# Kernel optimization log

Hardware: AMD Instinct MI355X
Metric: run time of the kernel (lower is better)

The kernel has to match this reference:

```python
import jax, jax.numpy as jnp
import numpy as np

N_NODES = 100000
N_EDGES = 3200000
IN_DIM = 128
HID = 128
K = 20  # n_gaussians


def gcn_conv(x, src, dst, W, b, n_nodes):
    """PyG GCNConv: add self-loops, symmetric normalization, linear transform.
    out = D^{-1/2} (A + I) D^{-1/2} (x @ W) + b, where D is degree of A+I.
    """
    h = x @ W  # [N, out_dim]
    # degree on A + I (self-loop contributes 1 to every node)
    deg = jax.ops.segment_sum(jnp.ones_like(dst, dtype=h.dtype), dst,
                              num_segments=n_nodes) + 1.0
    dis = jax.lax.rsqrt(deg)  # deg >= 1, safe
    norm = dis[src] * dis[dst]  # [E]
    # gather -> scale -> scatter-add (edges), plus self-loop term dis_i^2 * h_i
    agg = jax.ops.segment_sum(h[src] * norm[:, None], dst,
                              num_segments=n_nodes)
    agg = agg + h * (dis * dis)[:, None]
    return agg + b


def setup_inputs() -> dict:
    key = jax.random.key(0)
    ks = jax.random.split(key, 12)
    x = jax.random.normal(ks[0], (N_NODES, IN_DIM), dtype=jnp.float32)
    edge_index = jax.random.randint(ks[1], (2, N_EDGES), 0, N_NODES, dtype=jnp.int32)
    s = 1.0 / np.sqrt(HID)
    W1 = jax.random.uniform(ks[2], (IN_DIM, HID), jnp.float32, -s, s)
    b1 = jnp.zeros((HID,), jnp.float32)
    W2 = jax.random.uniform(ks[3], (HID, HID), jnp.float32, -s, s)
    b2 = jnp.zeros((HID,), jnp.float32)
    pi_W = jax.random.uniform(ks[4], (HID, K), jnp.float32, -s, s)
    pi_b = jnp.zeros((K,), jnp.float32)
    mu_W = jax.random.uniform(ks[5], (HID, K), jnp.float32, -s, s)
    mu_b = jnp.zeros((K,), jnp.float32)
    ls_W = jax.random.uniform(ks[6], (HID, K), jnp.float32, -s, s)
    ls_b = jnp.zeros((K,), jnp.float32)
    return {"x": x, "edge_index": edge_index, "W1": W1, "b1": b1,
            "W2": W2, "b2": b2, "pi_W": pi_W, "pi_b": pi_b,
            "mu_W": mu_W, "mu_b": mu_b, "ls_W": ls_W, "ls_b": ls_b}


def reference(x, edge_index, W1, b1, W2, b2, pi_W, pi_b, mu_W, mu_b, ls_W, ls_b):
    src, dst = edge_index[0], edge_index[1]
    n = x.shape[0]
    h = jax.nn.relu(gcn_conv(x, src, dst, W1, b1, n))
    h = jax.nn.relu(gcn_conv(h, src, dst, W2, b2, n))
    pi = jax.nn.softmax(h @ pi_W + pi_b, axis=1)
    mu = h @ mu_W + mu_b
    log_sigma = h @ ls_W + ls_b
    return (pi, mu, log_sigma)
```

## Files before the change

### kernel.cpp

```cpp
#include <hip/hip_runtime.h>
#include <hip/hip_fp16.h>
#include <cstdint>
#include <cstddef>

#define IN_DIM 128
#define HID    128
#define NG     20
#define T      4096
#define MAXB   400

typedef _Float16 half8 __attribute__((ext_vector_type(8)));
typedef _Float16 half4 __attribute__((ext_vector_type(4)));
typedef float    f32x4 __attribute__((ext_vector_type(4)));

__global__ void zero_ints(int* __restrict__ a, int n) {
  int i = blockIdx.x * blockDim.x + threadIdx.x;
  if (i < n) a[i] = 0;
}

__global__ __launch_bounds__(256) void binsort1(const int* __restrict__ src,
    const int* __restrict__ dst, int* __restrict__ tmp, int* __restrict__ bofs,
    int* __restrict__ bintot, int NBC, int E) {
  __shared__ int lhist[MAXB];
  __shared__ int lscan[512];
  __shared__ int lcur[MAXB];
  __shared__ int sbuf[T];
  int tid = threadIdx.x;
  int tile0 = blockIdx.x * T;
  int m = E - tile0; if (m > T) m = T;

  for (int i = tid; i < NBC; i += 256) lhist[i] = 0;
  __syncthreads();

  int dreg[16];
#pragma unroll
  for (int j = 0; j < 16; ++j) {
    int idx = j * 256 + tid;
    dreg[j] = -1;
    if (idx < m) {
      int d = dst[tile0 + idx];
      dreg[j] = d;
      atomicAdd(&lhist[d >> 8], 1);
    }
  }
  __syncthreads();

  int v0 = (tid < NBC) ? lhist[tid] : 0;
  int v1 = (256 + tid < NBC) ? lhist[256 + tid] : 0;
  lscan[tid] = v0; lscan[256 + tid] = v1;
  __syncthreads();
  for (int o = 1; o < 512; o <<= 1) {
    int a0 = (tid >= o) ? lscan[tid - o] : 0;
    int a1 = (256 + tid >= o) ? lscan[256 + tid - o] : 0;
    __syncthreads();
    lscan[tid] += a0; lscan[256 + tid] += a1;
    __syncthreads();
  }
  if (tid < NBC)       lcur[tid]       = lscan[tid] - v0;
  if (256 + tid < NBC) lcur[256 + tid] = lscan[256 + tid] - v1;
  __syncthreads();

  int ST = NBC + 1;
  for (int i = tid; i < NBC; i += 256) bofs[(size_t)blockIdx.x * ST + i] = lcur[i];
  if (tid == 0) bofs[(size_t)blockIdx.x * ST + NBC] = m;
  for (int i = tid; i < NBC; i += 256)
    if (lhist[i]) atomicAdd(&bintot[i], lhist[i]);
  __syncthreads();

#pragma unroll
  for (int j = 0; j < 16; ++j) {
    int idx = j * 256 + tid;
    if (idx < m) {
      int d = dreg[j];
      int s = src[tile0 + idx];
      int slot = atomicAdd(&lcur[d >> 8], 1);
      sbuf[slot] = ((d & 255) << 17) | s;
    }
  }
  __syncthreads();

  int nv = m >> 2;
  int4* out4 = (int4*)(tmp + tile0);
  const int4* sb4 = (const int4*)sbuf;
  for (int i = tid; i < nv; i += 256) out4[i] = sb4[i];
  for (int i = (nv << 2) + tid; i < m; i += 256) tmp[tile0 + i] = sbuf[i];
}

__global__ __launch_bounds__(512) void binscan(const int* __restrict__ bintot,
                                               int* __restrict__ binbase, int NBC) {
  __shared__ int s[512];
  int tid = threadIdx.x;
  int v = (tid < NBC) ? bintot[tid] : 0;
  s[tid] = v;
  __syncthreads();
  for (int o = 1; o < 512; o <<= 1) {
    int t = (tid >= o) ? s[tid - o] : 0;
    __syncthreads();
    s[tid] += t;
    __syncthreads();
  }
  if (tid < NBC) binbase[tid] = s[tid] - v;
}

__global__ __launch_bounds__(512) void binsort2(const int* __restrict__ tmp,
    const int* __restrict__ bofs, const int* __restrict__ binbase,
    int* __restrict__ csrc, int* __restrict__ cnt, float* __restrict__ dis,
    int* __restrict__ offs, int NBC, int nblk, int N) {
  __shared__ int lcnt[256];
  __shared__ int lsc[256];
  __shared__ int lcur2[256];
  int b = blockIdx.x;
  int tid = threadIdx.x;
  if (tid < 256) lcnt[tid] = 0;
  __syncthreads();
  int ST = NBC + 1;
  for (int r = tid; r < nblk; r += 512) {
    int s = bofs[(size_t)r * ST + b];
    int e2 = bofs[(size_t)r * ST + b + 1];
    int base = r * T;
    for (int k = s; k < e2; ++k)
      atomicAdd(&lcnt[tmp[base + k] >> 17], 1);
  }
  __syncthreads();
  if (tid < 256) lsc[tid] = lcnt[tid];
  __syncthreads();
  for (int o = 1; o < 256; o <<= 1) {
    int t = 0;
    if (tid < 256 && tid >= o) t = lsc[tid - o];
    __syncthreads();
    if (tid < 256) lsc[tid] += t;
    __syncthreads();
  }
  int gbase = binbase[b];
  if (tid < 256) {
    int excl = lsc[tid] - lcnt[tid];
    lcur2[tid] = gbase + excl;
    int node = (b << 8) + tid;
    if (node < N) {
      cnt[node] = lcnt[tid];
      dis[node] = rsqrtf((float)lcnt[tid] + 1.0f);
      offs[node] = gbase + excl;
    }
  }
  __syncthreads();
  for (int r = tid; r < nblk; r += 512) {
    int s = bofs[(size_t)r * ST + b];
    int e2 = bofs[(size_t)r * ST + b + 1];
    int base = r * T;
    for (int k = s; k < e2; ++k) {
      int rec = tmp[base + k];
      int pos = atomicAdd(&lcur2[rec >> 17], 1);
      csrc[pos] = rec & 0x1FFFF;
    }
  }
}

__global__ __launch_bounds__(256) void gemm128_mfma(const float* __restrict__ A,
                                                    const float* __restrict__ B,
                                                    __half* __restrict__ C, int M) {
  __shared__ _Float16 sA[128][136];
  const int tid = threadIdx.x;
  const int m0 = blockIdx.x * 128;

#pragma unroll
  for (int q = 0; q < 16; ++q) {
    int idx = q * 256 + tid;
    int r = idx >> 5;
    int cc = (idx & 31) << 2;
    float4 v = make_float4(0.f, 0.f, 0.f, 0.f);
    if (m0 + r < M) v = *(const float4*)(A + (size_t)(m0 + r) * 128 + cc);
    half4 hv;
    hv[0] = (_Float16)v.x; hv[1] = (_Float16)v.y;
    hv[2] = (_Float16)v.z; hv[3] = (_Float16)v.w;
    *(half4*)(&sA[r][cc]) = hv;
  }
  __syncthreads();

  const int wave = tid >> 6, lane = tid & 63;
  const int nbase = wave << 5;
  const int lrow = lane & 15;
  const int khi  = lane >> 4;

  half8 bf[2][4];
#pragma unroll
  for (int nf = 0; nf < 2; ++nf) {
    const float* wcol = B + (nbase + nf * 16 + lrow);
#pragma unroll
    for (int ks = 0; ks < 4; ++ks) {
      half8 hb;
#pragma unroll
      for (int rr = 0; rr < 8; ++rr)
        hb[rr] = (_Float16)wcol[(size_t)(ks * 32 + khi * 8 + rr) * 128];
      bf[nf][ks] = hb;
    }
  }

  f32x4 acc[8][2];
#pragma unroll
  for (int mf = 0; mf < 8; ++mf)
#pragma unroll
    for (int nf = 0; nf < 2; ++nf) acc[mf][nf] = (f32x4){0.f, 0.f, 0.f, 0.f};

#pragma unroll
  for (int mf = 0; mf < 8; ++mf) {
    const _Float16* ar = &sA[mf * 16 + lrow][khi * 8];
    half8 a0 = *(const half8*)(ar);
    half8 a1 = *(const half8*)(ar + 32);
    half8 a2 = *(const half8*)(ar + 64);
    half8 a3 = *(const half8*)(ar + 96);
    acc[mf][0] = __builtin_amdgcn_mfma_f32_16x16x32_f16(a0, bf[0][0], acc[mf][0], 0, 0, 0);
    acc[mf][1] = __builtin_amdgcn_mfma_f32_16x16x32_f16(a0, bf[1][0], acc[mf][1], 0, 0, 0);
    acc[mf][0] = __builtin_amdgcn_mfma_f32_16x16x32_f16(a1, bf[0][1], acc[mf][0], 0, 0, 0);
    acc[mf][1] = __builtin_amdgcn_mfma_f32_16x16x32_f16(a1, bf[1][1], acc[mf][1], 0, 0, 0);
    acc[mf][0] = __builtin_amdgcn_mfma_f32_16x16x32_f16(a2, bf[0][2], acc[mf][0], 0, 0, 0);
    acc[mf][1] = __builtin_amdgcn_mfma_f32_16x16x32_f16(a2, bf[1][2], acc[mf][1], 0, 0, 0);
    acc[mf][0] = __builtin_amdgcn_mfma_f32_16x16x32_f16(a3, bf[0][3], acc[mf][0], 0, 0, 0);
    acc[mf][1] = __builtin_amdgcn_mfma_f32_16x16x32_f16(a3, bf[1][3], acc[mf][1], 0, 0, 0);
  }

#pragma unroll
  for (int mf = 0; mf < 8; ++mf) {
    int r0 = mf * 16 + khi * 4;
#pragma unroll
    for (int nf = 0; nf < 2; ++nf) {
      int ccol = nbase + nf * 16 + lrow;
#pragma unroll
      for (int reg = 0; reg < 4; ++reg) {
        int r = m0 + r0 + reg;
        if (r < M) C[(size_t)r * 128 + ccol] = __float2half(acc[mf][nf][reg]);
      }
    }
  }
}

__global__ __launch_bounds__(256) void agg_kernel(const __half* __restrict__ h,
    const int* __restrict__ csrc,
    const int* __restrict__ offs, const int* __restrict__ cnt,
    const float* __restrict__ dis, const float* __restrict__ bias,
    float* __restrict__ out, int n) {
  int wave = threadIdx.x >> 6;
  int lane = threadIdx.x & 63;
  int i0 = (blockIdx.x * 4 + wave) * 2;
  if (i0 >= n) return;
  int i1 = i0 + 1;
  bool has1 = i1 < n;
  int c = lane * 2;

  int st0 = offs[i0];
  int m0  = cnt[i0];
  float d0 = dis[i0];
  int st1 = 0, m1 = 0;
  float d1 = 0.f;
  if (has1) { st1 = offs[i1]; m1 = cnt[i1]; d1 = dis[i1]; }

  float ax0 = 0.f, ay0 = 0.f, ax1 = 0.f, ay1 = 0.f;
  int mMax = m0 > m1 ? m0 : m1;

  for (int base = 0; base < mMax; base += 64) {
    int mcA = m0 - base; mcA = mcA < 0 ? 0 : (mcA > 64 ? 64 : mcA);
    int mcB = m1 - base; mcB = mcB < 0 ? 0 : (mcB > 64 ? 64 : mcB);
    int mc = mcA > mcB ? mcA : mcB;

    int sA = 0, sB = 0;
    float wA = 0.f, wB = 0.f;
    if (lane < mcA) sA = csrc[st0 + base + lane];
    if (lane < mcB) sB = csrc[st1 + base + lane];
    if (lane < mcA) wA = dis[sA] * d0;
    if (lane < mcB) wB = dis[sB] * d1;

    int j = 0;
    for (; j + 4 <= mc; j += 4) {
      int   a0 = __shfl(sA, j);
      int   a1 = __shfl(sA, j + 1);
      int   a2 = __shfl(sA, j + 2);
      int   a3 = __shfl(sA, j + 3);
      int   b0 = __shfl(sB, j);
      int   b1 = __shfl(sB, j + 1);
      int   b2 = __shfl(sB, j + 2);
      int   b3 = __shfl(sB, j + 3);
      float u0 = __shfl(wA, j);
      float u1 = __shfl(wA, j + 1);
      float u2 = __shfl(wA, j + 2);
      float u3 = __shfl(wA, j + 3);
      float v0 = __shfl(wB, j);
      float v1 = __shfl(wB, j + 1);
      float v2 = __shfl(wB, j + 2);
      float v3 = __shfl(wB, j + 3);
      float2 hA0 = __half22float2(*(const __half2*)(h + ((size_t)a0 << 7) + c));
      float2 hA1 = __half22float2(*(const __half2*)(h + ((size_t)a1 << 7) + c));
      float2 hA2 = __half22float2(*(const __half2*)(h + ((size_t)a2 << 7) + c));
      float2 hA3 = __half22float2(*(const __half2*)(h + ((size_t)a3 << 7) + c));
      float2 hB0 = __half22float2(*(const __half2*)(h + ((size_t)b0 << 7) + c));
      float2 hB1 = __half22float2(*(const __half2*)(h + ((size_t)b1 << 7) + c));
      float2 hB2 = __half22float2(*(const __half2*)(h + ((size_t)b2 << 7) + c));
      float2 hB3 = __half22float2(*(const __half2*)(h + ((size_t)b3 << 7) + c));
      ax0 = fmaf(hA0.x, u0, ax0); ay0 = fmaf(hA0.y, u0, ay0);
      ax0 = fmaf(hA1.x, u1, ax0); ay0 = fmaf(hA1.y, u1, ay0);
      ax0 = fmaf(hA2.x, u2, ax0); ay0 = fmaf(hA2.y, u2, ay0);
      ax0 = fmaf(hA3.x, u3, ax0); ay0 = fmaf(hA3.y, u3, ay0);
      ax1 = fmaf(hB0.x, v0, ax1); ay1 = fmaf(hB0.y, v0, ay1);
      ax1 = fmaf(hB1.x, v1, ax1); ay1 = fmaf(hB1.y, v1, ay1);
      ax1 = fmaf(hB2.x, v2, ax1); ay1 = fmaf(hB2.y, v2, ay1);
      ax1 = fmaf(hB3.x, v3, ax1); ay1 = fmaf(hB3.y, v3, ay1);
    }
    for (; j < mc; ++j) {
      int   a0 = __shfl(sA, j);
      int   b0 = __shfl(sB, j);
      float u0 = __shfl(wA, j);
      float v0 = __shfl(wB, j);
      float2 hA0 = __half22float2(*(const __half2*)(h + ((size_t)a0 << 7) + c));
      float2 hB0 = __half22float2(*(const __half2*)(h + ((size_t)b0 << 7) + c));
      ax0 = fmaf(hA0.x, u0, ax0); ay0 = fmaf(hA0.y, u0, ay0);
      ax1 = fmaf(hB0.x, v0, ax1); ay1 = fmaf(hB0.y, v0, ay1);
    }
  }

  float2 bv = *(const float2*)(bias + c);
  {
    float dd = d0 * d0;
    float2 hs = __half22float2(*(const __half2*)(h + ((size_t)i0 << 7) + c));
    float vx = fmaf(hs.x, dd, ax0) + bv.x;
    float vy = fmaf(hs.y, dd, ay0) + bv.y;
    *(float2*)(out + (size_t)i0 * 128 + c) = make_float2(fmaxf(vx, 0.f), fmaxf(vy, 0.f));
  }
  if (has1) {
    float dd = d1 * d1;
    float2 hs = __half22float2(*(const __half2*)(h + ((size_t)i1 << 7) + c));
    float vx = fmaf(hs.x, dd, ax1) + bv.x;
    float vy = fmaf(hs.y, dd, ay1) + bv.y;
    *(float2*)(out + (size_t)i1 * 128 + c) = make_float2(fmaxf(vx, 0.f), fmaxf(vy, 0.f));
  }
}

__global__ void pack_heads_w(const float* __restrict__ piW, const float* __restrict__ muW,
                             const float* __restrict__ lsW, float* __restrict__ W64) {
  int i = blockIdx.x * 256 + threadIdx.x;
  if (i >= 128 * 64) return;
  int k = i >> 6, j = i & 63;
  float v = 0.f;
  if (j < 20)      v = piW[k * 20 + j];
  else if (j < 40) v = muW[k * 20 + (j - 20)];
  else if (j < 60) v = lsW[k * 20 + (j - 40)];
  W64[i] = v;
}

#define KC 64
__global__ __launch_bounds__(256) void gemm_heads(const float* __restrict__ A,
                                                  const float* __restrict__ B,
                                                  float* __restrict__ C, int M) {
  __shared__ float sA[64][KC + 4];
  __shared__ float sB[KC][68];
  int tid = threadIdx.x;
  int m0 = blockIdx.x * 64;
  int tr = tid >> 4;
  int tc = tid & 15;
  float acc[4][4];
#pragma unroll
  for (int i = 0; i < 4; ++i)
#pragma unroll
    for (int j = 0; j < 4; ++j) acc[i][j] = 0.f;

  for (int k0 = 0; k0 < 128; k0 += KC) {
#pragma unroll
    for (int q = 0; q < 4; ++q) {
      int idx = q * 256 + tid;
      int r = idx >> 4;
      int kk = (idx & 15) << 2;
      float4 v = make_float4(0.f, 0.f, 0.f, 0.f);
      if (m0 + r < M) v = *(const float4*)(A + (size_t)(m0 + r) * 128 + k0 + kk);
      *(float4*)(&sA[r][kk]) = v;
    }
#pragma unroll
    for (int q = 0; q < 4; ++q) {
      int idx = q * 256 + tid;
      int kk = idx >> 4;
      int nn = (idx & 15) << 2;
      *(float4*)(&sB[kk][nn]) = *(const float4*)(B + (size_t)(k0 + kk) * 64 + nn);
    }
    __syncthreads();
#pragma unroll 4
    for (int k = 0; k < KC; k += 4) {
      float4 a0 = *(const float4*)(&sA[tr][k]);
      float4 a1 = *(const float4*)(&sA[tr + 16][k]);
      float4 a2 = *(const float4*)(&sA[tr + 32][k]);
      float4 a3 = *(const float4*)(&sA[tr + 48][k]);
#pragma unroll
      for (int u = 0; u < 4; ++u) {
        float4 b = *(const float4*)(&sB[k + u][tc * 4]);
        float av[4] = {((const float*)&a0)[u], ((const float*)&a1)[u],
                       ((const float*)&a2)[u], ((const float*)&a3)[u]};
#pragma unroll
        for (int i = 0; i < 4; ++i) {
          acc[i][0] = fmaf(av[i], b.x, acc[i][0]);
          acc[i][1] = fmaf(av[i], b.y, acc[i][1]);
          acc[i][2] = fmaf(av[i], b.z, acc[i][2]);
          acc[i][3] = fmaf(av[i], b.w, acc[i][3]);
        }
      }
    }
    __syncthreads();
  }
#pragma unroll
  for (int i = 0; i < 4; ++i) {
    int r = m0 + tr + 16 * i;
    if (r < M)
      *(float4*)(C + (size_t)r * 64 + tc * 4) =
          make_float4(acc[i][0], acc[i][1], acc[i][2], acc[i][3]);
  }
}

__global__ __launch_bounds__(256) void heads_post(const float* __restrict__ out60,
    const float* __restrict__ pib, const float* __restrict__ mub,
    const float* __restrict__ lsb, float* __restrict__ out, int n) {
  int wave = threadIdx.x >> 6, lane = threadIdx.x & 63;
  int node = blockIdx.x * 4 + wave;
  if (node >= n) return;
  float v = 0.f;
  if (lane < 60) {
    v = out60[(size_t)node * 64 + lane];
    v += (lane < 20) ? pib[lane] : (lane < 40) ? mub[lane - 20] : lsb[lane - 40];
  }
  float pv = (lane < 20) ? v : -__builtin_inff();
  float mx = pv;
  for (int o = 16; o > 0; o >>= 1) mx = fmaxf(mx, __shfl_down(mx, o, 32));
  mx = __shfl(mx, 0, 32);
  float ev = (lane < 20) ? expf(v - mx) : 0.f;
  float sm = ev;
  for (int o = 16; o > 0; o >>= 1) sm += __shfl_down(sm, o, 32);
  sm = __shfl(sm, 0, 32);

  size_t base = (size_t)n * NG;
  if (lane < 20)      out[(size_t)node * NG + lane] = ev / sm;
  else if (lane < 40) out[base + (size_t)node * NG + (lane - 20)] = v;
  else if (lane < 60) out[2 * base + (size_t)node * NG + (lane - 40)] = v;
}

extern "C" void kernel_launch(void* const* d_in, const int* in_sizes, int n_in,
                              void* d_out, int out_size, void* d_ws, size_t ws_size,
                              hipStream_t stream) {
  const float* x   = (const float*)d_in[0];
  const int*   ei  = (const int*)d_in[1];
  const float* W1  = (const float*)d_in[2];
  const float* b1  = (const float*)d_in[3];
  const float* W2  = (const float*)d_in[4];
  const float* b2  = (const float*)d_in[5];
  const float* piW = (const float*)d_in[6];
  const float* pib = (const float*)d_in[7];
  const float* muW = (const float*)d_in[8];
  const float* mub = (const float*)d_in[9];
  const float* lsW = (const float*)d_in[10];
  const float* lsb = (const float*)d_in[11];
  float* out = (float*)d_out;

  const int N = in_sizes[0] / IN_DIM;
  const int E = in_sizes[1] / 2;
  const int* src = ei;
  const int* dst = ei + E;

  const int NBC  = (N + 255) >> 8;
  const int nblk = (E + T - 1) / T;
  const int ST   = NBC + 1;

  char* p = (char*)d_ws;
  char* regionH = p;                        p += (size_t)N * HID * sizeof(__half);
  __half* h16  = (__half*)regionH;
  float* out60 = (float*)regionH;
  char* regionR = p;
  size_t szR = (size_t)N * HID * sizeof(float);
  size_t szT = (size_t)E * sizeof(int);
  p += (szR > szT ? szR : szT);
  int*   tmp    = (int*)regionR;
  float* bufB   = (float*)regionR;
  int*   csrc   = (int*)p;                  p += (size_t)E * sizeof(int);
  int*   bofs   = (int*)p;                  p += (size_t)nblk * ST * sizeof(int);
  int*   bintot = (int*)p;                  p += (size_t)MAXB * sizeof(int);
  int*   binbase= (int*)p;                  p += (size_t)MAXB * sizeof(int);
  int*   cnt    = (int*)p;                  p += (size_t)N * sizeof(int);
  int*   offs   = (int*)p;                  p += (size_t)N * sizeof(int);
  float* dis    = (float*)p;                p += (size_t)N * sizeof(float);
  float* W64    = (float*)p;                p += (size_t)128 * 64 * sizeof(float);

  zero_ints<<<(NBC + 255) / 256, 256, 0, stream>>>(bintot, NBC);
  binsort1<<<nblk, 256, 0, stream>>>(src, dst, tmp, bofs, bintot, NBC, E);
  binscan<<<1, 512, 0, stream>>>(bintot, binbase, NBC);
  binsort2<<<NBC, 512, 0, stream>>>(tmp, bofs, binbase, csrc, cnt, dis, offs,
                                    NBC, nblk, N);
  pack_heads_w<<<(128 * 64 + 255) / 256, 256, 0, stream>>>(piW, muW, lsW, W64);

  const int NB8  = (N + 7) / 8;
  const int NBG  = (N + 127) / 128;

  gemm128_mfma<<<NBG, 256, 0, stream>>>(x, W1, h16, N);
  agg_kernel<<<NB8, 256, 0, stream>>>(h16, csrc, offs, cnt, dis, b1, bufB, N);
  gemm128_mfma<<<NBG, 256, 0, stream>>>(bufB, W2, h16, N);
  agg_kernel<<<NB8, 256, 0, stream>>>(h16, csrc, offs, cnt, dis, b2, bufB, N);

  gemm_heads<<<(N + 63) / 64, 256, 0, stream>>>(bufB, W64, out60, N);
  heads_post<<<(N + 3) / 4, 256, 0, stream>>>(out60, pib, mub, lsb, out, N);
}
```

Baseline: 548.9 us.

## Split aggregation into feature chunks with 8 edges gathered in parallel per wave

The aggregation kernel is restructured so each block handles one 16-column feature chunk, with a grid eight times larger. Within a wave, 8 lane groups each gather a different edge's 32-byte chunk, and the partial sums are combined with an xor-shuffle reduction. The aim is more memory-level parallelism and more blocks for the irregular gather. In exchange, the neighbour indices, weights and dis lookups are now fetched once per chunk, eight times in total, and each gather is only 32 bytes wide.

Measured after the change: 1.048 ms. +91.0%, slower.

```diff
diff --git a/kernel.cpp b/kernel.cpp
--- a/kernel.cpp
+++ b/kernel.cpp
@@ -233,24 +233,28 @@
   }
 }
 
-__global__ __launch_bounds__(256) void agg_kernel(const __half* __restrict__ h,
-    const int* __restrict__ csrc,
-    const int* __restrict__ offs, const int* __restrict__ cnt,
-    const float* __restrict__ dis, const float* __restrict__ bias,
-    float* __restrict__ out, int n) {
-  int wave = threadIdx.x >> 6;
-  int lane = threadIdx.x & 63;
-  int i0 = (blockIdx.x * 4 + wave) * 2;
+#define NCHUNK 8
+#define CHW    16
+__global__ __launch_bounds__(256) void agg_pass(const __half* __restrict__ h,
+    const int* __restrict__ csrc, const int* __restrict__ offs,
+    const int* __restrict__ cnt, const float* __restrict__ dis,
+    const float* __restrict__ bias, float* __restrict__ out,
+    int n, int nodeBlocks) {
+  const int chunk = blockIdx.x / nodeBlocks;
+  const int nb    = blockIdx.x % nodeBlocks;
+  const int wave  = threadIdx.x >> 6;
+  const int lane  = threadIdx.x & 63;
+  const int g = lane >> 3;
+  const int l = lane & 7;
+  const int c = chunk * CHW + l * 2;
+
+  int i0 = (nb * 4 + wave) * 2;
   if (i0 >= n) return;
   int i1 = i0 + 1;
   bool has1 = i1 < n;
-  int c = lane * 2;
-
-  int st0 = offs[i0];
-  int m0  = cnt[i0];
-  float d0 = dis[i0];
-  int st1 = 0, m1 = 0;
-  float d1 = 0.f;
+
+  int st0 = offs[i0]; int m0 = cnt[i0]; float d0 = dis[i0];
+  int st1 = 0, m1 = 0; float d1 = 0.f;
   if (has1) { st1 = offs[i1]; m1 = cnt[i1]; d1 = dis[i1]; }
 
   float ax0 = 0.f, ay0 = 0.f, ax1 = 0.f, ay1 = 0.f;
@@ -268,62 +272,35 @@
     if (lane < mcA) wA = dis[sA] * d0;
     if (lane < mcB) wB = dis[sB] * d1;
 
-    int j = 0;
-    for (; j + 4 <= mc; j += 4) {
-      int   a0 = __shfl(sA, j);
-      int   a1 = __shfl(sA, j + 1);
-      int   a2 = __shfl(sA, j + 2);
-      int   a3 = __shfl(sA, j + 3);
-      int   b0 = __shfl(sB, j);
-      int   b1 = __shfl(sB, j + 1);
-      int   b2 = __shfl(sB, j + 2);
-      int   b3 = __shfl(sB, j + 3);
-      float u0 = __shfl(wA, j);
-      float u1 = __shfl(wA, j + 1);
-      float u2 = __shfl(wA, j + 2);
-      float u3 = __shfl(wA, j + 3);
-      float v0 = __shfl(wB, j);
-      float v1 = __shfl(wB, j + 1);
-      float v2 = __shfl(wB, j + 2);
-      float v3 = __shfl(wB, j + 3);
-      float2 hA0 = __half22float2(*(const __half2*)(h + ((size_t)a0 << 7) + c));
-      float2 hA1 = __half22float2(*(const __half2*)(h + ((size_t)a1 << 7) + c));
-      float2 hA2 = __half22float2(*(const __half2*)(h + ((size_t)a2 << 7) + c));
-      float2 hA3 = __half22float2(*(const __half2*)(h + ((size_t)a3 << 7) + c));
-      float2 hB0 = __half22float2(*(const __half2*)(h + ((size_t)b0 << 7) + c));
-      float2 hB1 = __half22float2(*(const __half2*)(h + ((size_t)b1 << 7) + c));
-      float2 hB2 = __half22float2(*(const __half2*)(h + ((size_t)b2 << 7) + c));
-      float2 hB3 = __half22float2(*(const __half2*)(h + ((size_t)b3 << 7) + c));
-      ax0 = fmaf(hA0.x, u0, ax0); ay0 = fmaf(hA0.y, u0, ay0);
-      ax0 = fmaf(hA1.x, u1, ax0); ay0 = fmaf(hA1.y, u1, ay0);
-      ax0 = fmaf(hA2.x, u2, ax0); ay0 = fmaf(hA2.y, u2, ay0);
-      ax0 = fmaf(hA3.x, u3, ax0); ay0 = fmaf(hA3.y, u3, ay0);
-      ax1 = fmaf(hB0.x, v0, ax1); ay1 = fmaf(hB0.y, v0, ay1);
-      ax1 = fmaf(hB1.x, v1, ax1); ay1 = fmaf(hB1.y, v1, ay1);
-      ax1 = fmaf(hB2.x, v2, ax1); ay1 = fmaf(hB2.y, v2, ay1);
-      ax1 = fmaf(hB3.x, v3, ax1); ay1 = fmaf(hB3.y, v3, ay1);
-    }
-    for (; j < mc; ++j) {
-      int   a0 = __shfl(sA, j);
-      int   b0 = __shfl(sB, j);
-      float u0 = __shfl(wA, j);
-      float v0 = __shfl(wB, j);
-      float2 hA0 = __half22float2(*(const __half2*)(h + ((size_t)a0 << 7) + c));
-      float2 hB0 = __half22float2(*(const __half2*)(h + ((size_t)b0 << 7) + c));
-      ax0 = fmaf(hA0.x, u0, ax0); ay0 = fmaf(hA0.y, u0, ay0);
-      ax1 = fmaf(hB0.x, v0, ax1); ay1 = fmaf(hB0.y, v0, ay1);
-    }
+    for (int j = 0; j < mc; j += 8) {
+      int idx = j + g;
+      int   ea = __shfl(sA, idx);
+      float ua = __shfl(wA, idx);
+      int   eb = __shfl(sB, idx);
+      float ub = __shfl(wB, idx);
+      float2 ha = __half22float2(*(const __half2*)(h + ((size_t)ea << 7) + c));
+      float2 hb = __half22float2(*(const __half2*)(h + ((size_t)eb << 7) + c));
+      ax0 = fmaf(ha.x, ua, ax0); ay0 = fmaf(ha.y, ua, ay0);
+      ax1 = fmaf(hb.x, ub, ax1); ay1 = fmaf(hb.y, ub, ay1);
+    }
+  }
+
+#pragma unroll
+  for (int off = 8; off < 64; off <<= 1) {
+    ax0 += __shfl_xor(ax0, off);
+    ay0 += __shfl_xor(ay0, off);
+    ax1 += __shfl_xor(ax1, off);
+    ay1 += __shfl_xor(ay1, off);
   }
 
   float2 bv = *(const float2*)(bias + c);
-  {
+  if (g == 0) {
     float dd = d0 * d0;
     float2 hs = __half22float2(*(const __half2*)(h + ((size_t)i0 << 7) + c));
     float vx = fmaf(hs.x, dd, ax0) + bv.x;
     float vy = fmaf(hs.y, dd, ay0) + bv.y;
     *(float2*)(out + (size_t)i0 * 128 + c) = make_float2(fmaxf(vx, 0.f), fmaxf(vy, 0.f));
-  }
-  if (has1) {
+  } else if (g == 1 && has1) {
     float dd = d1 * d1;
     float2 hs = __half22float2(*(const __half2*)(h + ((size_t)i1 << 7) + c));
     float vx = fmaf(hs.x, dd, ax1) + bv.x;
@@ -487,13 +464,14 @@
                                     NBC, nblk, N);
   pack_heads_w<<<(128 * 64 + 255) / 256, 256, 0, stream>>>(piW, muW, lsW, W64);
 
-  const int NB8  = (N + 7) / 8;
+  const int nodeBlocks = (N + 7) / 8;
+  const int NBAgg = nodeBlocks * NCHUNK;
   const int NBG  = (N + 127) / 128;
 
   gemm128_mfma<<<NBG, 256, 0, stream>>>(x, W1, h16, N);
-  agg_kernel<<<NB8, 256, 0, stream>>>(h16, csrc, offs, cnt, dis, b1, bufB, N);
+  agg_pass<<<NBAgg, 256, 0, stream>>>(h16, csrc, offs, cnt, dis, b1, bufB, N, nodeBlocks);
   gemm128_mfma<<<NBG, 256, 0, stream>>>(bufB, W2, h16, N);
-  agg_kernel<<<NB8, 256, 0, stream>>>(h16, csrc, offs, cnt, dis, b2, bufB, N);
+  agg_pass<<<NBAgg, 256, 0, stream>>>(h16, csrc, offs, cnt, dis, b2, bufB, N, nodeBlocks);
 
   gemm_heads<<<(N + 63) / 64, 256, 0, stream>>>(bufB, W64, out60, N);
   heads_post<<<(N + 3) / 4, 256, 0, stream>>>(out60, pib, mub, lsb, out, N);
```

## Replace two-pass bin sort CSR build with global atomic count-scan-scatter

Applied to the files above, without the earlier changes.

Swaps the tiled two-level bin sort (shared-memory local sort plus per-bin second pass) for a plain CSR build: global atomic degree count, block-local scan plus bin scan, then a global atomic scatter of source ids. This removes the tmp staging buffer and the serial per-bin loops in binsort2, which ran one block per 256 nodes. In exchange it relies on 3.2M global atomics to random addresses twice. Neighbour order within a row also becomes nondeterministic, which changes gather locality and the order of the float summation.

Result: slower. 779.0 us (+41.9%).

```diff
diff --git a/kernel.cpp b/kernel.cpp
--- a/kernel.cpp
+++ b/kernel.cpp
@@ -6,7 +6,6 @@
 #define IN_DIM 128
 #define HID    128
 #define NG     20
-#define T      4096
 #define MAXB   400
 
 typedef _Float16 half8 __attribute__((ext_vector_type(8)));
@@ -18,72 +17,32 @@
   if (i < n) a[i] = 0;
 }
 
-__global__ __launch_bounds__(256) void binsort1(const int* __restrict__ src,
-    const int* __restrict__ dst, int* __restrict__ tmp, int* __restrict__ bofs,
-    int* __restrict__ bintot, int NBC, int E) {
-  __shared__ int lhist[MAXB];
-  __shared__ int lscan[512];
-  __shared__ int lcur[MAXB];
-  __shared__ int sbuf[T];
+__global__ __launch_bounds__(256) void count_deg(const int* __restrict__ dst,
+                                                 int* __restrict__ cnt, int E) {
+  int e0 = (blockIdx.x * 256 + threadIdx.x) * 4;
+#pragma unroll
+  for (int j = 0; j < 4; ++j) {
+    int e = e0 + j;
+    if (e < E) atomicAdd(&cnt[dst[e]], 1);
+  }
+}
+
+__global__ __launch_bounds__(256) void scan_local(const int* __restrict__ cnt,
+    int* __restrict__ offs, int* __restrict__ bsum, int N) {
+  __shared__ int s[256];
   int tid = threadIdx.x;
-  int tile0 = blockIdx.x * T;
-  int m = E - tile0; if (m > T) m = T;
-
-  for (int i = tid; i < NBC; i += 256) lhist[i] = 0;
+  int node = blockIdx.x * 256 + tid;
+  int v = (node < N) ? cnt[node] : 0;
+  s[tid] = v;
   __syncthreads();
-
-  int dreg[16];
-#pragma unroll
-  for (int j = 0; j < 16; ++j) {
-    int idx = j * 256 + tid;
-    dreg[j] = -1;
-    if (idx < m) {
-      int d = dst[tile0 + idx];
-      dreg[j] = d;
-      atomicAdd(&lhist[d >> 8], 1);
-    }
-  }
-  __syncthreads();
-
-  int v0 = (tid < NBC) ? lhist[tid] : 0;
-  int v1 = (256 + tid < NBC) ? lhist[256 + tid] : 0;
-  lscan[tid] = v0; lscan[256 + tid] = v1;
-  __syncthreads();
-  for (int o = 1; o < 512; o <<= 1) {
-    int a0 = (tid >= o) ? lscan[tid - o] : 0;
-    int a1 = (256 + tid >= o) ? lscan[256 + tid - o] : 0;
-    __syncthreads();
-    lscan[tid] += a0; lscan[256 + tid] += a1;
-    __syncthreads();
-  }
-  if (tid < NBC)       lcur[tid]       = lscan[tid] - v0;
-  if (256 + tid < NBC) lcur[256 + tid] = lscan[256 + tid] - v1;
-  __syncthreads();
-
-  int ST = NBC + 1;
-  for (int i = tid; i < NBC; i += 256) bofs[(size_t)blockIdx.x * ST + i] = lcur[i];
-  if (tid == 0) bofs[(size_t)blockIdx.x * ST + NBC] = m;
-  for (int i = tid; i < NBC; i += 256)
-    if (lhist[i]) atomicAdd(&bintot[i], lhist[i]);
-  __syncthreads();
-
-#pragma unroll
-  for (int j = 0; j < 16; ++j) {
-    int idx = j * 256 + tid;
-    if (idx < m) {
-      int d = dreg[j];
-      int s = src[tile0 + idx];
-      int slot = atomicAdd(&lcur[d >> 8], 1);
-      sbuf[slot] = ((d & 255) << 17) | s;
-    }
-  }
-  __syncthreads();
-
-  int nv = m >> 2;
-  int4* out4 = (int4*)(tmp + tile0);
-  const int4* sb4 = (const int4*)sbuf;
-  for (int i = tid; i < nv; i += 256) out4[i] = sb4[i];
-  for (int i = (nv << 2) + tid; i < m; i += 256) tmp[tile0 + i] = sbuf[i];
+  for (int o = 1; o < 256; o <<= 1) {
+    int t = (tid >= o) ? s[tid - o] : 0;
+    __syncthreads();
+    s[tid] += t;
+    __syncthreads();
+  }
+  if (node < N) offs[node] = s[tid] - v;
+  if (tid == 255) bsum[blockIdx.x] = s[255];
 }
 
 __global__ __launch_bounds__(512) void binscan(const int* __restrict__ bintot,
@@ -102,55 +61,29 @@
   if (tid < NBC) binbase[tid] = s[tid] - v;
 }
 
-__global__ __launch_bounds__(512) void binsort2(const int* __restrict__ tmp,
-    const int* __restrict__ bofs, const int* __restrict__ binbase,
-    int* __restrict__ csrc, int* __restrict__ cnt, float* __restrict__ dis,
-    int* __restrict__ offs, int NBC, int nblk, int N) {
-  __shared__ int lcnt[256];
-  __shared__ int lsc[256];
-  __shared__ int lcur2[256];
-  int b = blockIdx.x;
-  int tid = threadIdx.x;
-  if (tid < 256) lcnt[tid] = 0;
-  __syncthreads();
-  int ST = NBC + 1;
-  for (int r = tid; r < nblk; r += 512) {
-    int s = bofs[(size_t)r * ST + b];
-    int e2 = bofs[(size_t)r * ST + b + 1];
-    int base = r * T;
-    for (int k = s; k < e2; ++k)
-      atomicAdd(&lcnt[tmp[base + k] >> 17], 1);
-  }
-  __syncthreads();
-  if (tid < 256) lsc[tid] = lcnt[tid];
-  __syncthreads();
-  for (int o = 1; o < 256; o <<= 1) {
-    int t = 0;
-    if (tid < 256 && tid >= o) t = lsc[tid - o];
-    __syncthreads();
-    if (tid < 256) lsc[tid] += t;
-    __syncthreads();
-  }
-  int gbase = binbase[b];
-  if (tid < 256) {
-    int excl = lsc[tid] - lcnt[tid];
-    lcur2[tid] = gbase + excl;
-    int node = (b << 8) + tid;
-    if (node < N) {
-      cnt[node] = lcnt[tid];
-      dis[node] = rsqrtf((float)lcnt[tid] + 1.0f);
-      offs[node] = gbase + excl;
-    }
-  }
-  __syncthreads();
-  for (int r = tid; r < nblk; r += 512) {
-    int s = bofs[(size_t)r * ST + b];
-    int e2 = bofs[(size_t)r * ST + b + 1];
-    int base = r * T;
-    for (int k = s; k < e2; ++k) {
-      int rec = tmp[base + k];
-      int pos = atomicAdd(&lcur2[rec >> 17], 1);
-      csrc[pos] = rec & 0x1FFFF;
+__global__ __launch_bounds__(256) void finalize_meta(const int* __restrict__ cnt,
+    int* __restrict__ offs, int* __restrict__ gcur, float* __restrict__ dis,
+    const int* __restrict__ binbase, int N) {
+  int node = blockIdx.x * 256 + threadIdx.x;
+  if (node >= N) return;
+  int o = offs[node] + binbase[node >> 8];
+  offs[node] = o;
+  gcur[node] = o;
+  dis[node] = rsqrtf((float)cnt[node] + 1.0f);
+}
+
+__global__ __launch_bounds__(256) void scatter_csr(const int* __restrict__ src,
+    const int* __restrict__ dst, int* __restrict__ gcur,
+    int* __restrict__ csrc, int E) {
+  int e0 = (blockIdx.x * 256 + threadIdx.x) * 4;
+#pragma unroll
+  for (int j = 0; j < 4; ++j) {
+    int e = e0 + j;
+    if (e < E) {
+      int d = dst[e];
+      int s = src[e];
+      int pos = atomicAdd(&gcur[d], 1);
+      csrc[pos] = s;
     }
   }
 }
@@ -457,38 +390,32 @@
   const int* src = ei;
   const int* dst = ei + E;
 
-  const int NBC  = (N + 255) >> 8;
-  const int nblk = (E + T - 1) / T;
-  const int ST   = NBC + 1;
+  const int NBC = (N + 255) >> 8;
 
   char* p = (char*)d_ws;
   char* regionH = p;                        p += (size_t)N * HID * sizeof(__half);
   __half* h16  = (__half*)regionH;
   float* out60 = (float*)regionH;
-  char* regionR = p;
-  size_t szR = (size_t)N * HID * sizeof(float);
-  size_t szT = (size_t)E * sizeof(int);
-  p += (szR > szT ? szR : szT);
-  int*   tmp    = (int*)regionR;
-  float* bufB   = (float*)regionR;
+  float* bufB  = (float*)p;                 p += (size_t)N * HID * sizeof(float);
   int*   csrc   = (int*)p;                  p += (size_t)E * sizeof(int);
-  int*   bofs   = (int*)p;                  p += (size_t)nblk * ST * sizeof(int);
-  int*   bintot = (int*)p;                  p += (size_t)MAXB * sizeof(int);
+  int*   bsum   = (int*)p;                  p += (size_t)MAXB * sizeof(int);
   int*   binbase= (int*)p;                  p += (size_t)MAXB * sizeof(int);
   int*   cnt    = (int*)p;                  p += (size_t)N * sizeof(int);
   int*   offs   = (int*)p;                  p += (size_t)N * sizeof(int);
+  int*   gcur   = (int*)p;                  p += (size_t)N * sizeof(int);
   float* dis    = (float*)p;                p += (size_t)N * sizeof(float);
   float* W64    = (float*)p;                p += (size_t)128 * 64 * sizeof(float);
 
-  zero_ints<<<(NBC + 255) / 256, 256, 0, stream>>>(bintot, NBC);
-  binsort1<<<nblk, 256, 0, stream>>>(src, dst, tmp, bofs, bintot, NBC, E);
-  binscan<<<1, 512, 0, stream>>>(bintot, binbase, NBC);
-  binsort2<<<NBC, 512, 0, stream>>>(tmp, bofs, binbase, csrc, cnt, dis, offs,
-                                    NBC, nblk, N);
+  zero_ints<<<(N + 255) / 256, 256, 0, stream>>>(cnt, N);
+  count_deg<<<(E / 4 + 255) / 256, 256, 0, stream>>>(dst, cnt, E);
+  scan_local<<<NBC, 256, 0, stream>>>(cnt, offs, bsum, N);
+  binscan<<<1, 512, 0, stream>>>(bsum, binbase, NBC);
+  finalize_meta<<<(N + 255) / 256, 256, 0, stream>>>(cnt, offs, gcur, dis, binbase, N);
+  scatter_csr<<<(E / 4 + 255) / 256, 256, 0, stream>>>(src, dst, gcur, csrc, E);
   pack_heads_w<<<(128 * 64 + 255) / 256, 256, 0, stream>>>(piW, muW, lsW, W64);
 
-  const int NB8  = (N + 7) / 8;
-  const int NBG  = (N + 127) / 128;
+  const int NB8 = (N + 7) / 8;
+  const int NBG = (N + 127) / 128;
 
   gemm128_mfma<<<NBG, 256, 0, stream>>>(x, W1, h16, N);
   agg_kernel<<<NB8, 256, 0, stream>>>(h16, csrc, offs, cnt, dis, b1, bufB, N);
```
